# Performance work log

Measured on AMD Instinct MI355X. Metric: run time of the kernel, lower is better.

The kernel has to match this reference:

```python
import jax, jax.numpy as jnp
import numpy as np

T, B, NHID = 64, 32, 768
NB, BS = 6, 128          # num_blocks, block_size = nhid // num_blocks
TOPK = 4                 # active blocks per step
NTOK = 32000
ATT = 4 * BS             # input-attention value dim (att_out), per RIMs BlocksCore
DK = 64                  # input-attention key dim
NH2, DK2 = 4, 16         # communication attention heads / head dim


def setup_inputs() -> dict:
    key = jax.random.key(0)
    ks = jax.random.split(key, 16)
    s = 0.02
    return {
        "x": jax.random.normal(ks[0], (T, B, NHID), jnp.float32),
        "hx0": jax.random.normal(ks[1], (B, NHID), jnp.float32),
        "cx0": jax.random.normal(ks[2], (B, NHID), jnp.float32),
        # input attention (1 head): per-read-block query proj, per-write-slot key/value proj
        "Wq_in": jax.random.normal(ks[3], (NB, BS, DK), jnp.float32) * s,
        "Wk_in": jax.random.normal(ks[4], (2, NHID, DK), jnp.float32) * s,
        "Wv_in": jax.random.normal(ks[5], (2, NHID, ATT), jnp.float32) * s,
        # block-diagonal LSTM (blockify_params): per-block weights
        "Wih": jax.random.normal(ks[6], (NB, ATT, 4 * BS), jnp.float32) * s,
        "Whh": jax.random.normal(ks[7], (NB, BS, 4 * BS), jnp.float32) * s,
        "b_lstm": jnp.zeros((NB, 4 * BS), jnp.float32),
        # communication attention (4 heads, dk=dv=16), per-block projections + output proj
        "Wq_c": jax.random.normal(ks[8], (NB, BS, NH2 * DK2), jnp.float32) * s,
        "Wk_c": jax.random.normal(ks[9], (NB, BS, NH2 * DK2), jnp.float32) * s,
        "Wv_c": jax.random.normal(ks[10], (NB, BS, NH2 * DK2), jnp.float32) * s,
        "Wo_c": jax.random.normal(ks[11], (NB, NH2 * DK2, BS), jnp.float32) * s,
        # decoder
        "Wd": jax.random.normal(ks[12], (NTOK, NHID), jnp.float32) * 0.1,
        "bd": jnp.zeros((NTOK,), jnp.float32),
    }


def _step(hx, cx, xt, Wq_in, Wk_in, Wv_in, Wih, Whh, b_lstm, Wq_c, Wk_c, Wv_c, Wo_c):
    hb = hx.reshape(B, NB, BS)
    cb = cx.reshape(B, NB, BS)
    # --- input attention: each block reads from {null, input} slots ---
    kv_in = jnp.stack([jnp.zeros_like(xt), xt], axis=1)          # [B,2,NHID]
    q = jnp.einsum('bnd,ndk->bnk', hb, Wq_in)                    # [B,NB,DK]
    k = jnp.einsum('bmd,mdk->bmk', kv_in, Wk_in)                 # [B,2,DK]
    v = jnp.einsum('bmd,mdv->bmv', kv_in, Wv_in)                 # [B,2,ATT]
    iatt = jax.nn.softmax(
        jnp.einsum('bnk,bmk->bnm', q, k) / jnp.sqrt(jnp.float32(DK)), axis=-1)
    inp_use = jnp.einsum('bnm,bmv->bnv', iatt, v)                # [B,NB,ATT]
    # --- top-k block routing: drop NB-TOPK blocks attending most to null ---
    null_att = iatt[:, :, 0]                                     # [B,NB]
    _, drop_idx = jax.lax.top_k(null_att, NB - TOPK)
    mask = jnp.ones((B, NB), hx.dtype).at[
        jnp.arange(B)[:, None], drop_idx].set(0.0)               # [B,NB]
    # --- per-block (block-diagonal) LSTM ---
    gates = (jnp.einsum('bnv,nvg->bng', inp_use, Wih)
             + jnp.einsum('bnh,nhg->bng', hb, Whh) + b_lstm)     # [B,NB,4*BS]
    i, f, g, o = jnp.split(gates, 4, axis=-1)
    c_new = jax.nn.sigmoid(f) * cb + jax.nn.sigmoid(i) * jnp.tanh(g)
    h_new = jax.nn.sigmoid(o) * jnp.tanh(c_new)                  # [B,NB,BS]
    # --- communication attention among blocks (residual) ---
    q2 = jnp.einsum('bnd,ndk->bnk', h_new, Wq_c).reshape(B, NB, NH2, DK2)
    k2 = jnp.einsum('bnd,ndk->bnk', h_new, Wk_c).reshape(B, NB, NH2, DK2)
    v2 = jnp.einsum('bnd,ndk->bnk', h_new, Wv_c).reshape(B, NB, NH2, DK2)
    att = jax.nn.softmax(
        jnp.einsum('bihk,bjhk->bhij', q2, k2) / jnp.sqrt(jnp.float32(DK2)), axis=-1)
    comm = jnp.einsum('bhij,bjhv->bihv', att, v2).reshape(B, NB, NH2 * DK2)
    h_new = h_new + jnp.einsum('bnk,nkd->bnd', comm, Wo_c)
    # --- gated state update: inactive blocks keep old state ---
    m = mask[:, :, None]
    hx_next = (m * h_new + (1.0 - m) * hb).reshape(B, NHID)
    cx_next = (m * c_new + (1.0 - m) * cb).reshape(B, NHID)
    return hx_next, cx_next


def reference(x, hx0, cx0, Wq_in, Wk_in, Wv_in, Wih, Whh, b_lstm,
              Wq_c, Wk_c, Wv_c, Wo_c, Wd, bd):
    def scan_step(carry, xt):
        hx, cx = carry
        hx, cx = _step(hx, cx, xt, Wq_in, Wk_in, Wv_in, Wih, Whh, b_lstm,
                       Wq_c, Wk_c, Wv_c, Wo_c)
        return (hx, cx), hx
    (hx, cx), outs = jax.lax.scan(scan_step, (hx0, cx0), x)     # outs: [T,B,NHID]
    decoded = outs.reshape(T * B, NHID) @ Wd.T + bd              # [T*B,NTOK]
    return decoded, hx, cx
```

## Files before the change

kernel.cpp:

```cpp
#include <hip/hip_runtime.h>
#include <hip/hip_bf16.h>
#include <stdint.h>

#define TT 64
#define BB 32
#define NHIDC 768
#define NBK 6
#define BSZ 128
#define NTOKC 32000

using f32x4  = __attribute__((ext_vector_type(4))) float;
using f32x2  = __attribute__((ext_vector_type(2))) float;
using short8 = __attribute__((ext_vector_type(8))) short;
typedef unsigned long long u64;

#define OFF_XPUB  4096u
#define OFF_HTB   8065024u
#define OFF_K1    11210752u
#define OFF_V1    11735040u
#define OFF_U     15929344u
#define OFF_WDB   41095168u

__device__ __forceinline__ float sigf(float x){ return 1.f/(1.f + expf(-x)); }

__device__ __forceinline__ void stp(u64* p, float v, unsigned tag){
  union { float f; unsigned u; } cv; cv.f = v;
  const u64 pk = ((u64)tag << 32) | cv.u;
  __hip_atomic_store(p, pk, __ATOMIC_RELAXED, __HIP_MEMORY_SCOPE_AGENT);
}
__device__ __forceinline__ float ldp(const u64* p, unsigned tag){
  u64 v = __hip_atomic_load(p, __ATOMIC_RELAXED, __HIP_MEMORY_SCOPE_AGENT);
  while ((unsigned)(v >> 32) < tag){
    __builtin_amdgcn_s_sleep(1);
    v = __hip_atomic_load(p, __ATOMIC_RELAXED, __HIP_MEMORY_SCOPE_AGENT);
  }
  union { unsigned u; float f; } cv; cv.u = (unsigned)v;
  return cv.f;
}
#define CBAR asm volatile("" ::: "memory")

__device__ __forceinline__ void gload16(const void* g, void* l){
  __builtin_amdgcn_global_load_lds(
      (const __attribute__((address_space(1))) unsigned int*)g,
      (__attribute__((address_space(3))) unsigned int*)l, 16, 0, 0);
}

__device__ __forceinline__ int xslot(int par, int gg, int nn, int b){
  return (((par*16 + gg)*6 + nn)*2 + b)*132;
}

__global__ void prep_kernel(const float* __restrict__ Wd,
                            unsigned short* __restrict__ Wdb,
                            u64* __restrict__ xpub)
{
  {
    int i = blockIdx.x*blockDim.x + threadIdx.x;
    const int nx = 2*16*6*2*132;
    const int stride = gridDim.x*blockDim.x;
    for (; i < nx; i += stride)
      __hip_atomic_store(xpub + i, 0ull, __ATOMIC_RELAXED, __HIP_MEMORY_SCOPE_AGENT);
  }
  int i = blockIdx.x*blockDim.x + threadIdx.x;
  const int n4 = NTOKC*NHIDC/4;
  const int stride = gridDim.x*blockDim.x;
  for (; i < n4; i += stride){
    const float4 v = ((const float4*)Wd)[i];
    ushort4 o;
    __hip_bfloat16 b0 = __float2bfloat16(v.x); o.x = *reinterpret_cast<unsigned short*>(&b0);
    __hip_bfloat16 b1 = __float2bfloat16(v.y); o.y = *reinterpret_cast<unsigned short*>(&b1);
    __hip_bfloat16 b2 = __float2bfloat16(v.z); o.z = *reinterpret_cast<unsigned short*>(&b2);
    __hip_bfloat16 b3 = __float2bfloat16(v.w); o.w = *reinterpret_cast<unsigned short*>(&b3);
    ((ushort4*)Wdb)[i] = o;
  }
}

template<int TM, int TN>
__global__ __launch_bounds__(256) void gemm_f32(
    const float* __restrict__ A, int lda,
    const float* __restrict__ B, int ldb, long bstride,
    float* __restrict__ C, int ldc, long cstride,
    int N, int K)
{
  constexpr int BM = 16*TM, BN = 16*TN;
  __shared__ float As[16][BM];
  __shared__ float Bs[16][BN+4];
  const float* Bb = B + (long)blockIdx.z * bstride;
  float* Cb = C + (long)blockIdx.z * cstride;
  const int m0 = blockIdx.x*BM, n0 = blockIdx.y*BN;
  const int tid = threadIdx.x, tx = tid & 15, ty = tid >> 4;
  float acc[TM][TN];
  #pragma unroll
  for (int i=0;i<TM;++i)
    #pragma unroll
    for (int j=0;j<TN;++j) acc[i][j]=0.f;

  for (int k0=0; k0<K; k0+=16){
    if constexpr (TM == 8){
      const int r = tid>>1, kk = (tid&1)*8;
      const float4 v0 = *(const float4*)&A[(long)(m0+r)*lda + k0 + kk];
      const float4 v1 = *(const float4*)&A[(long)(m0+r)*lda + k0 + kk + 4];
      As[kk+0][r]=v0.x; As[kk+1][r]=v0.y; As[kk+2][r]=v0.z; As[kk+3][r]=v0.w;
      As[kk+4][r]=v1.x; As[kk+5][r]=v1.y; As[kk+6][r]=v1.z; As[kk+7][r]=v1.w;
    } else {
      const int r = tid>>2, kk = (tid&3)*4;
      const float4 v0 = *(const float4*)&A[(long)(m0+r)*lda + k0 + kk];
      As[kk+0][r]=v0.x; As[kk+1][r]=v0.y; As[kk+2][r]=v0.z; As[kk+3][r]=v0.w;
    }
    if constexpr (TN == 8){
      const int rb = tid>>4, cb = (tid&15)*8;
      float4 v0 = {0,0,0,0}, v1 = {0,0,0,0};
      if (n0+cb+4 <= N) v0 = *(const float4*)&Bb[(long)(k0+rb)*ldb + n0+cb];
      if (n0+cb+8 <= N) v1 = *(const float4*)&Bb[(long)(k0+rb)*ldb + n0+cb+4];
      *(float4*)&Bs[rb][cb]   = v0;
      *(float4*)&Bs[rb][cb+4] = v1;
    } else {
      const int rb = tid>>4, cb = (tid&15)*4;
      float4 v0 = {0,0,0,0};
      if (n0+cb+4 <= N) v0 = *(const float4*)&Bb[(long)(k0+rb)*ldb + n0+cb];
      *(float4*)&Bs[rb][cb] = v0;
    }
    __syncthreads();
    #pragma unroll
    for (int kk=0; kk<16; ++kk){
      float av[TM], bv[TN];
      #pragma unroll
      for (int i=0;i<TM;++i) av[i] = As[kk][ty*TM+i];
      #pragma unroll
      for (int j=0;j<TN;++j) bv[j] = Bs[kk][tx*TN+j];
      #pragma unroll
      for (int i=0;i<TM;++i)
        #pragma unroll
        for (int j=0;j<TN;++j) acc[i][j] += av[i]*bv[j];
    }
    __syncthreads();
  }
  #pragma unroll
  for (int i=0;i<TM;++i){
    const int row = m0 + ty*TM + i;
    #pragma unroll
    for (int j=0;j<TN;++j){
      const int col = n0 + tx*TN + j;
      if (col < N) Cb[(long)row*ldc + col] = acc[i][j];
    }
  }
}

__global__ __launch_bounds__(1024, 2) void recurrent_kernel(
    const float* __restrict__ hx0, const float* __restrict__ cx0,
    const float* __restrict__ Wq_in, const float* __restrict__ Whh,
    const float* __restrict__ b_lstm,
    const float* __restrict__ Wk_c, const float* __restrict__ Wv_c,
    const float* __restrict__ Wq_c, const float* __restrict__ Wo_c,
    const float* __restrict__ K1buf, const float* __restrict__ Ubuf,
    u64* __restrict__ xpub,
    unsigned short* __restrict__ HTx,
    float* __restrict__ out_hx, float* __restrict__ out_cx)
{
  const int w = blockIdx.x, gg = w/6, n = w - gg*6, tid = threadIdx.x;

  __shared__ float WcT[192*130];
  __shared__ float WqL[128*65];
  __shared__ float hL[2][128], cL[2][128], h0L[2][128], cnL[2][128];
  __shared__ float partL[2][2][512];
  __shared__ float uL[2][512];
  __shared__ float blL[512];
  __shared__ float kvqL[2][192];
  __shared__ float kvAll[2][6][130];
  __shared__ float commL[2][64];
  __shared__ float nullAll[2][8];
  __shared__ float sL[2], nullLoc[2], maskL[2];

  const int kh = tid >> 9, gc = tid & 511;
  const int od = tid >> 3, okq = tid & 7;

  f32x4 whr[16];
  {
    const float* src = Whh + (long)n*65536 + kh*64*512 + gc;
    #pragma unroll
    for (int r4=0; r4<16; ++r4){
      f32x4 v;
      v[0] = src[(r4*4+0)*512]; v[1] = src[(r4*4+1)*512];
      v[2] = src[(r4*4+2)*512]; v[3] = src[(r4*4+3)*512];
      whr[r4] = v;
    }
  }
  #pragma unroll
  for (int i=0;i<16;++i) asm volatile("" : "+v"(whr[i]));
  f32x4 wo0, wo1;
  {
    const float* src = Wo_c + n*8192 + od;
    #pragma unroll
    for (int j=0;j<4;++j) wo0[j] = src[(okq*8+j)*128];
    #pragma unroll
    for (int j=0;j<4;++j) wo1[j] = src[(okq*8+4+j)*128];
  }
  asm volatile("" : "+v"(wo0));
  asm volatile("" : "+v"(wo1));

  if (tid < 512) blL[tid] = b_lstm[n*512 + tid];
  for (int i = tid; i < 8192; i += 1024){
    const int h = i>>6, c = i&63;
    WcT[(c    )*130 + h] = Wk_c[n*8192 + i];
    WcT[(c+ 64)*130 + h] = Wv_c[n*8192 + i];
    WcT[(c+128)*130 + h] = Wq_c[n*8192 + i];
    WqL[h*65 + c] = Wq_in[n*8192 + i];
  }
  if (tid < 256){
    const int b = tid>>7, d = tid&127;
    hL[b][d] = hx0[(gg*2+b)*768 + n*128 + d];
    cL[b][d] = cx0[(gg*2+b)*768 + n*128 + d];
  }
  __syncthreads();

  for (int t = 0; t < TT; ++t){
    const int par = t & 1;
    const unsigned tag = (unsigned)(t+1);
    uL[kh][gc] = Ubuf[((long)(t*32 + gg*2 + kh)*6 + n)*512 + gc];
    float k1r = 0.f;
    if (tid < 128) k1r = K1buf[(long)(t*32 + gg*2 + (tid>>6))*64 + (tid&63)];

    {
      float gd0 = 0.f, gd1 = 0.f;
      #pragma unroll
      for (int r4 = 0; r4 < 16; ++r4){
        const f32x4 h0v = *(const f32x4*)&hL[0][kh*64 + r4*4];
        const f32x4 h1v = *(const f32x4*)&hL[1][kh*64 + r4*4];
        #pragma unroll
        for (int j=0;j<4;++j){
          gd0 += whr[r4][j]*h0v[j];
          gd1 += whr[r4][j]*h1v[j];
        }
      }
      partL[0][kh][gc] = gd0;
      partL[1][kh][gc] = gd1;
    }
    if (tid < 128){
      const int b = tid>>6, k = tid&63;
      float q = 0.f;
      #pragma unroll 16
      for (int h=0; h<128; ++h) q += WqL[h*65 + k]*hL[b][h];
      float term = q*k1r;
      #pragma unroll
      for (int off=32; off; off>>=1) term += __shfl_xor(term, off);
      if (k == 0){
        const float l1 = term*0.125f;
        const float mx = fmaxf(l1, 0.f);
        const float e0 = expf(0.f-mx), e1 = expf(l1-mx);
        const float inv = 1.f/(e0+e1);
        sL[b] = e1*inv;
        nullLoc[b] = e0*inv;
        stp(xpub + xslot(par,gg,n,b) + 128, e0*inv, tag);
      }
    }
    __syncthreads();
    if (tid < 256){
      const int b = tid>>7, dd = tid&127;
      const float s = sL[b];
      const float gi = partL[b][0][dd]     + partL[b][1][dd]     + s*uL[b][dd]     + blL[dd];
      const float gf = partL[b][0][128+dd] + partL[b][1][128+dd] + s*uL[b][128+dd] + blL[128+dd];
      const float gG = partL[b][0][256+dd] + partL[b][1][256+dd] + s*uL[b][256+dd] + blL[256+dd];
      const float go = partL[b][0][384+dd] + partL[b][1][384+dd] + s*uL[b][384+dd] + blL[384+dd];
      const float cp = cL[b][dd];
      const float cn = sigf(gf)*cp + sigf(gi)*tanhf(gG);
      const float h0 = sigf(go)*tanhf(cn);
      cnL[b][dd] = cn; h0L[b][dd] = h0;
    }
    __syncthreads();
    if (tid < 384){
      const int b = tid/192, c = tid%192;
      float a = 0.f;
      #pragma unroll
      for (int h4=0; h4<32; ++h4){
        const f32x2 wa = *(const f32x2*)&WcT[c*130 + h4*4];
        const f32x2 wb = *(const f32x2*)&WcT[c*130 + h4*4 + 2];
        const f32x4 hv = *(const f32x4*)&h0L[b][h4*4];
        a += wa[0]*hv[0] + wa[1]*hv[1] + wb[0]*hv[2] + wb[1]*hv[3];
      }
      kvqL[b][c] = a;
      if (c < 128) stp(xpub + xslot(par,gg,n,b) + c, a, tag);
    }
    __syncthreads();
    for (int idx = tid; idx < 1536; idx += 1024){
      const int j = idx/256, r = idx&255, b = r>>7, c = r&127;
      if (j == n) kvAll[b][j][c] = kvqL[b][c];
      else        kvAll[b][j][c] = ldp(xpub + xslot(par,gg,j,b) + c, tag);
    }
    if (tid < 12){
      const int j = tid>>1, b = tid&1;
      if (j == n) nullAll[b][j] = nullLoc[b];
      else        nullAll[b][j] = ldp(xpub + xslot(par,gg,j,b) + 128, tag);
    }
    __syncthreads(); CBAR;
    if (tid < 64){
      const int lane = tid;
      const int g5 = lane>>3, l3 = lane&7;
      const int b = g5>>2, h = g5&3;
      float lg = -1e30f;
      if (l3 < 6){
        float s = 0.f;
        #pragma unroll
        for (int kk=0; kk<16; ++kk)
          s += kvqL[b][128 + h*16 + kk]*kvAll[b][l3][h*16 + kk];
        lg = s*0.25f;
      }
      float mx = lg;
      mx = fmaxf(mx, __shfl_xor(mx,1));
      mx = fmaxf(mx, __shfl_xor(mx,2));
      mx = fmaxf(mx, __shfl_xor(mx,4));
      float ev = (l3 < 6) ? expf(lg - mx) : 0.f;
      float sum = ev;
      sum += __shfl_xor(sum,1); sum += __shfl_xor(sum,2); sum += __shfl_xor(sum,4);
      const float myw = ev/sum;
      float s0 = 0.f, s1 = 0.f;
      #pragma unroll
      for (int j=0;j<6;++j){
        const float wj = __shfl(myw, g5*8 + j);
        s0 += wj*kvAll[b][j][64 + h*16 + l3*2];
        s1 += wj*kvAll[b][j][64 + h*16 + l3*2 + 1];
      }
      commL[b][h*16 + l3*2]     = s0;
      commL[b][h*16 + l3*2 + 1] = s1;
      if (lane < 2){
        const float own = nullAll[lane][n];
        int rank = 0;
        #pragma unroll
        for (int j=0;j<6;++j){
          const float v = nullAll[lane][j];
          rank += (v > own || (v == own && j < n)) ? 1 : 0;
        }
        maskL[lane] = (rank < 2) ? 0.f : 1.f;
      }
    }
    __syncthreads();
    {
      #pragma unroll
      for (int b=0; b<2; ++b){
        float a = 0.f;
        #pragma unroll
        for (int j=0;j<4;++j) a += commL[b][okq*8+j]*wo0[j];
        #pragma unroll
        for (int j=0;j<4;++j) a += commL[b][okq*8+4+j]*wo1[j];
        a += __shfl_xor(a,1); a += __shfl_xor(a,2); a += __shfl_xor(a,4);
        if (okq == 0 && maskL[b] != 0.f){
          hL[b][od] = h0L[b][od] + a;
          cL[b][od] = cnL[b][od];
        }
      }
    }
    __syncthreads();
    if (tid < 256){
      const int b = tid>>7, d = tid&127;
      const float hv = hL[b][d];
      __hip_bfloat16 hb16 = __float2bfloat16(hv);
      HTx[(long)(t*32 + gg*2 + b)*768 + n*128 + d] = *reinterpret_cast<unsigned short*>(&hb16);
      if (t == TT-1){
        out_hx[(gg*2+b)*768 + n*128 + d] = hv;
        out_cx[(gg*2+b)*768 + n*128 + d] = cL[b][d];
      }
    }
  }
}

__global__ __launch_bounds__(256) void decoder_kernel(
    const unsigned short* __restrict__ A,
    const unsigned short* __restrict__ Bw,
    const float* __restrict__ bd,
    float* __restrict__ out)
{
  __shared__ unsigned short As[4096];
  __shared__ unsigned short Bs[4096];
  const int bid = blockIdx.x;
  const int tile = (bid & 7)*500 + (bid >> 3);
  const int m0 = (tile & 15)*128, n0 = (tile >> 4)*128;
  const int tid = threadIdx.x;
  const int wv = tid >> 6, lane = tid & 63;
  const int wm = wv >> 1, wn = wv & 1;
  const int r16 = lane & 15, krow = lane >> 4;

  f32x4 acc[4][4] = {};

  for (int k0 = 0; k0 < 768; k0 += 32){
    #pragma unroll
    for (int i=0; i<2; ++i){
      const int idx = i*256 + tid;
      const int row = idx >> 2, k8 = (idx & 3)*8;
      gload16(&A [(long)(m0+row)*768 + k0 + k8], (char*)As + i*4096 + wv*1024);
      gload16(&Bw[(long)(n0+row)*768 + k0 + k8], (char*)Bs + i*4096 + wv*1024);
    }
    __syncthreads();
    short8 af[4], bf[4];
    #pragma unroll
    for (int mi=0; mi<4; ++mi)
      af[mi] = *(const short8*)&As[(wm*64 + mi*16 + r16)*32 + krow*8];
    #pragma unroll
    for (int ni=0; ni<4; ++ni)
      bf[ni] = *(const short8*)&Bs[(wn*64 + ni*16 + r16)*32 + krow*8];
    #pragma unroll
    for (int mi=0; mi<4; ++mi)
      #pragma unroll
      for (int ni=0; ni<4; ++ni)
        acc[mi][ni] = __builtin_amdgcn_mfma_f32_16x16x32_bf16(af[mi], bf[ni], acc[mi][ni], 0, 0, 0);
    __syncthreads();
  }

  #pragma unroll
  for (int ni=0; ni<4; ++ni){
    const int col = n0 + wn*64 + ni*16 + r16;
    const float bv = bd[col];
    #pragma unroll
    for (int mi=0; mi<4; ++mi){
      const int rbase = m0 + wm*64 + mi*16 + krow*4;
      #pragma unroll
      for (int j=0; j<4; ++j)
        out[(size_t)(rbase + j)*NTOKC + col] = acc[mi][ni][j] + bv;
    }
  }
}

extern "C" void kernel_launch(void* const* d_in, const int* in_sizes, int n_in,
                              void* d_out, int out_size, void* d_ws, size_t ws_size,
                              hipStream_t stream)
{
  (void)in_sizes; (void)n_in; (void)out_size; (void)ws_size;
  const float* x      = (const float*)d_in[0];
  const float* hx0    = (const float*)d_in[1];
  const float* cx0    = (const float*)d_in[2];
  const float* Wq_in  = (const float*)d_in[3];
  const float* Wk_in  = (const float*)d_in[4];
  const float* Wv_in  = (const float*)d_in[5];
  const float* Wih    = (const float*)d_in[6];
  const float* Whh    = (const float*)d_in[7];
  const float* b_lstm = (const float*)d_in[8];
  const float* Wq_c   = (const float*)d_in[9];
  const float* Wk_c   = (const float*)d_in[10];
  const float* Wv_c   = (const float*)d_in[11];
  const float* Wo_c   = (const float*)d_in[12];
  const float* Wd     = (const float*)d_in[13];
  const float* bd     = (const float*)d_in[14];

  char* ws = (char*)d_ws;
  u64*           xpub = (u64*)(ws + OFF_XPUB);
  unsigned short* HTx = (unsigned short*)(ws + OFF_HTB);
  float*         K1b  = (float*)(ws + OFF_K1);
  float*         V1b  = (float*)(ws + OFF_V1);
  float*         Ub   = (float*)(ws + OFF_U);
  unsigned short* Wdb = (unsigned short*)(ws + OFF_WDB);

  float* out_dec = (float*)d_out;
  float* out_hx  = out_dec + (size_t)2048*NTOKC;
  float* out_cx  = out_hx + BB*NHIDC;

  prep_kernel<<<2048, 256, 0, stream>>>(Wd, Wdb, xpub);
  gemm_f32<4,4><<<dim3(32,1,1), 256, 0, stream>>>(x, NHIDC, Wk_in + 768*64, 64, 0,
                                                  K1b, 64, 0, 64, NHIDC);
  gemm_f32<4,4><<<dim3(32,8,1), 256, 0, stream>>>(x, NHIDC, Wv_in + 768*512, 512, 0,
                                                  V1b, 512, 0, 512, NHIDC);
  gemm_f32<8,8><<<dim3(16,4,6), 256, 0, stream>>>(V1b, 512, Wih, 512, (long)512*512,
                                                  Ub, 3072, 512, 512, 512);
  recurrent_kernel<<<96, 1024, 0, stream>>>(hx0, cx0, Wq_in, Whh, b_lstm,
                                            Wk_c, Wv_c, Wq_c, Wo_c,
                                            K1b, Ub, xpub, HTx,
                                            out_hx, out_cx);
  decoder_kernel<<<4000, 256, 0, stream>>>(HTx, Wdb, bd, out_dec);
}
```

Before: 1.273 ms.

## Merge preprocessing GEMMs into two launches and widen decoder K-tile with swizzle

Four prep launches (weight conversion, xpub clear, K/V projections, Wih GEMM) become two kernels. Each kernel partitions its blocks between independent jobs, so fewer launches are serialized and the bf16 Wd conversion overlaps the Wih GEMM. Separately, the decoder GEMM now stages a K-tile of 64 instead of 32, using an XOR-swizzled LDS layout to avoid bank conflicts. That halves the barriers per K-loop and doubles LDS per block, which may lower occupancy.

```diff
diff --git a/kernel.cpp b/kernel.cpp
--- a/kernel.cpp
+++ b/kernel.cpp
@@ -49,45 +49,17 @@
   return (((par*16 + gg)*6 + nn)*2 + b)*132;
 }
 
-__global__ void prep_kernel(const float* __restrict__ Wd,
-                            unsigned short* __restrict__ Wdb,
-                            u64* __restrict__ xpub)
-{
-  {
-    int i = blockIdx.x*blockDim.x + threadIdx.x;
-    const int nx = 2*16*6*2*132;
-    const int stride = gridDim.x*blockDim.x;
-    for (; i < nx; i += stride)
-      __hip_atomic_store(xpub + i, 0ull, __ATOMIC_RELAXED, __HIP_MEMORY_SCOPE_AGENT);
-  }
-  int i = blockIdx.x*blockDim.x + threadIdx.x;
-  const int n4 = NTOKC*NHIDC/4;
-  const int stride = gridDim.x*blockDim.x;
-  for (; i < n4; i += stride){
-    const float4 v = ((const float4*)Wd)[i];
-    ushort4 o;
-    __hip_bfloat16 b0 = __float2bfloat16(v.x); o.x = *reinterpret_cast<unsigned short*>(&b0);
-    __hip_bfloat16 b1 = __float2bfloat16(v.y); o.y = *reinterpret_cast<unsigned short*>(&b1);
-    __hip_bfloat16 b2 = __float2bfloat16(v.z); o.z = *reinterpret_cast<unsigned short*>(&b2);
-    __hip_bfloat16 b3 = __float2bfloat16(v.w); o.w = *reinterpret_cast<unsigned short*>(&b3);
-    ((ushort4*)Wdb)[i] = o;
-  }
-}
-
 template<int TM, int TN>
-__global__ __launch_bounds__(256) void gemm_f32(
-    const float* __restrict__ A, int lda,
-    const float* __restrict__ B, int ldb, long bstride,
-    float* __restrict__ C, int ldc, long cstride,
-    int N, int K)
+__device__ void gemm_tile(const float* __restrict__ A, int lda,
+                          const float* __restrict__ Bb, int ldb,
+                          float* __restrict__ Cb, int ldc,
+                          int N, int K, int m0, int n0,
+                          float* AsP, float* BsP, int tid)
 {
   constexpr int BM = 16*TM, BN = 16*TN;
-  __shared__ float As[16][BM];
-  __shared__ float Bs[16][BN+4];
-  const float* Bb = B + (long)blockIdx.z * bstride;
-  float* Cb = C + (long)blockIdx.z * cstride;
-  const int m0 = blockIdx.x*BM, n0 = blockIdx.y*BN;
-  const int tid = threadIdx.x, tx = tid & 15, ty = tid >> 4;
+  float (*As)[BM]   = reinterpret_cast<float(*)[BM]>(AsP);
+  float (*Bs)[BN+4] = reinterpret_cast<float(*)[BN+4]>(BsP);
+  const int tx = tid & 15, ty = tid >> 4;
   float acc[TM][TN];
   #pragma unroll
   for (int i=0;i<TM;++i)
@@ -145,6 +117,56 @@
   }
 }
 
+__global__ __launch_bounds__(256) void pre1_kernel(
+    const float* __restrict__ x,
+    const float* __restrict__ Wk_in, const float* __restrict__ Wv_in,
+    float* __restrict__ K1b, float* __restrict__ V1b,
+    u64* __restrict__ xpub)
+{
+  __shared__ float As[16*128];
+  __shared__ float Bs[16*132];
+  const int bid = blockIdx.x, tid = threadIdx.x;
+  if (bid < 32){
+    gemm_tile<4,4>(x, 768, Wk_in + 768*64, 64, K1b, 64, 64, 768,
+                   bid*64, 0, As, Bs, tid);
+  } else if (bid < 288){
+    const int v = bid - 32;
+    gemm_tile<4,4>(x, 768, Wv_in + 768*512, 512, V1b, 512, 512, 768,
+                   (v>>3)*64, (v&7)*64, As, Bs, tid);
+  } else {
+    const int nx = 2*16*6*2*132;
+    for (int i = (bid-288)*256 + tid; i < nx; i += 64*256)
+      __hip_atomic_store(&xpub[i], 0ull, __ATOMIC_RELAXED, __HIP_MEMORY_SCOPE_AGENT);
+  }
+}
+
+__global__ __launch_bounds__(256) void pre2_kernel(
+    const float* __restrict__ V1b, const float* __restrict__ Wih,
+    const float* __restrict__ Wd,
+    float* __restrict__ Ub, unsigned short* __restrict__ Wdb)
+{
+  __shared__ float As[16*128];
+  __shared__ float Bs[16*132];
+  const int bid = blockIdx.x, tid = threadIdx.x;
+  if (bid < 384){
+    const int m = bid/24, r = bid%24, nt = r/6, z = r%6;
+    gemm_tile<8,8>(V1b, 512, Wih + (long)z*262144, 512,
+                   Ub + (long)z*512, 3072, 512, 512, m*128, nt*128,
+                   As, Bs, tid);
+  } else {
+    const long n4 = (long)NTOKC*NHIDC/4;
+    for (long i = (long)(bid-384)*256 + tid; i < n4; i += (long)512*256){
+      const float4 v = ((const float4*)Wd)[i];
+      ushort4 o;
+      __hip_bfloat16 b0 = __float2bfloat16(v.x); o.x = *reinterpret_cast<unsigned short*>(&b0);
+      __hip_bfloat16 b1 = __float2bfloat16(v.y); o.y = *reinterpret_cast<unsigned short*>(&b1);
+      __hip_bfloat16 b2 = __float2bfloat16(v.z); o.z = *reinterpret_cast<unsigned short*>(&b2);
+      __hip_bfloat16 b3 = __float2bfloat16(v.w); o.w = *reinterpret_cast<unsigned short*>(&b3);
+      ((ushort4*)Wdb)[i] = o;
+    }
+  }
+}
+
 __global__ __launch_bounds__(1024, 2) void recurrent_kernel(
     const float* __restrict__ hx0, const float* __restrict__ cx0,
     const float* __restrict__ Wq_in, const float* __restrict__ Whh,
@@ -367,8 +389,8 @@
     const float* __restrict__ bd,
     float* __restrict__ out)
 {
-  __shared__ unsigned short As[4096];
-  __shared__ unsigned short Bs[4096];
+  __shared__ unsigned short As[8192];
+  __shared__ unsigned short Bs[8192];
   const int bid = blockIdx.x;
   const int tile = (bid & 7)*500 + (bid >> 3);
   const int m0 = (tile & 15)*128, n0 = (tile >> 4)*128;
@@ -379,27 +401,42 @@
 
   f32x4 acc[4][4] = {};
 
-  for (int k0 = 0; k0 < 768; k0 += 32){
-    #pragma unroll
-    for (int i=0; i<2; ++i){
+  for (int k0 = 0; k0 < 768; k0 += 64){
+    #pragma unroll
+    for (int i=0; i<4; ++i){
       const int idx = i*256 + tid;
-      const int row = idx >> 2, k8 = (idx & 3)*8;
-      gload16(&A [(long)(m0+row)*768 + k0 + k8], (char*)As + i*4096 + wv*1024);
-      gload16(&Bw[(long)(n0+row)*768 + k0 + k8], (char*)Bs + i*4096 + wv*1024);
-    }
-    __syncthreads();
-    short8 af[4], bf[4];
+      const int row = idx >> 3, cp = idx & 7;
+      const int csrc = cp ^ (row & 7);
+      gload16(&A [(long)(m0+row)*768 + k0 + csrc*8], (char*)As + i*4096 + wv*1024);
+      gload16(&Bw[(long)(n0+row)*768 + k0 + csrc*8], (char*)Bs + i*4096 + wv*1024);
+    }
+    __syncthreads();
+    short8 af[4][2], bf[4][2];
+    #pragma unroll
+    for (int mi=0; mi<4; ++mi){
+      const int row = wm*64 + mi*16 + r16;
+      #pragma unroll
+      for (int ks=0; ks<2; ++ks){
+        const int kc = ks*4 + krow;
+        af[mi][ks] = *(const short8*)&As[row*64 + ((kc ^ (row&7))<<3)];
+      }
+    }
+    #pragma unroll
+    for (int ni=0; ni<4; ++ni){
+      const int row = wn*64 + ni*16 + r16;
+      #pragma unroll
+      for (int ks=0; ks<2; ++ks){
+        const int kc = ks*4 + krow;
+        bf[ni][ks] = *(const short8*)&Bs[row*64 + ((kc ^ (row&7))<<3)];
+      }
+    }
     #pragma unroll
     for (int mi=0; mi<4; ++mi)
-      af[mi] = *(const short8*)&As[(wm*64 + mi*16 + r16)*32 + krow*8];
-    #pragma unroll
-    for (int ni=0; ni<4; ++ni)
-      bf[ni] = *(const short8*)&Bs[(wn*64 + ni*16 + r16)*32 + krow*8];
-    #pragma unroll
-    for (int mi=0; mi<4; ++mi)
-      #pragma unroll
-      for (int ni=0; ni<4; ++ni)
-        acc[mi][ni] = __builtin_amdgcn_mfma_f32_16x16x32_bf16(af[mi], bf[ni], acc[mi][ni], 0, 0, 0);
+      #pragma unroll
+      for (int ni=0; ni<4; ++ni){
+        acc[mi][ni] = __builtin_amdgcn_mfma_f32_16x16x32_bf16(af[mi][0], bf[ni][0], acc[mi][ni], 0, 0, 0);
+        acc[mi][ni] = __builtin_amdgcn_mfma_f32_16x16x32_bf16(af[mi][1], bf[ni][1], acc[mi][ni], 0, 0, 0);
+      }
     __syncthreads();
   }
 
@@ -450,13 +487,8 @@
   float* out_hx  = out_dec + (size_t)2048*NTOKC;
   float* out_cx  = out_hx + BB*NHIDC;
 
-  prep_kernel<<<2048, 256, 0, stream>>>(Wd, Wdb, xpub);
-  gemm_f32<4,4><<<dim3(32,1,1), 256, 0, stream>>>(x, NHIDC, Wk_in + 768*64, 64, 0,
-                                                  K1b, 64, 0, 64, NHIDC);
-  gemm_f32<4,4><<<dim3(32,8,1), 256, 0, stream>>>(x, NHIDC, Wv_in + 768*512, 512, 0,
-                                                  V1b, 512, 0, 512, NHIDC);
-  gemm_f32<8,8><<<dim3(16,4,6), 256, 0, stream>>>(V1b, 512, Wih, 512, (long)512*512,
-                                                  Ub, 3072, 512, 512, 512);
+  pre1_kernel<<<352, 256, 0, stream>>>(x, Wk_in, Wv_in, K1b, V1b, xpub);
+  pre2_kernel<<<896, 256, 0, stream>>>(V1b, Wih, Wd, Ub, Wdb);
   recurrent_kernel<<<96, 1024, 0, stream>>>(hx0, cx0, Wq_in, Whh, b_lstm,
                                             Wk_c, Wv_c, Wq_c, Wo_c,
                                             K1b, Ub, xpub, HTx,
```

After: 1.219 ms. 4.3% less time.
